# Performance work log

Hardware: AMD Instinct MI355X
Metric: run time of the kernel (lower is better)

Reference implementation:

```python
import jax, jax.numpy as jnp
import numpy as np

NUM_EMBED = 54012  # hardcoded self.num_nodes in GraphNet
IN_FEATS = 256
HID = 32           # hardcoded gcn1 output width
OUT_FEATS = 256
N_NODES = 65536
N_EDGES = 1048576
BATCH = 4096


def setup_inputs() -> dict:
    key = jax.random.key(0)
    ks = jax.random.split(key, 12)
    # graph structure (int args)
    idx = jax.random.randint(ks[0], (N_NODES,), 0, NUM_EMBED)
    src = jax.random.randint(ks[1], (N_EDGES,), 0, N_NODES)
    dst = jax.random.randint(ks[2], (N_EDGES,), 0, N_NODES)
    gene1_idx = jax.random.randint(ks[3], (BATCH,), 0, N_NODES)
    gene2_idx = jax.random.randint(ks[4], (BATCH,), 0, N_NODES)
    # learned parameters (xavier-ish scaling)
    embed = jax.random.normal(ks[5], (NUM_EMBED, IN_FEATS), jnp.float32) * (2.0 / (NUM_EMBED + IN_FEATS)) ** 0.5
    W1 = jax.random.normal(ks[6], (IN_FEATS, HID), jnp.float32) * (2.0 / (IN_FEATS + HID)) ** 0.5
    b1 = jnp.zeros((HID,), jnp.float32)
    W2 = jax.random.normal(ks[7], (HID, OUT_FEATS), jnp.float32) * (2.0 / (HID + OUT_FEATS)) ** 0.5
    b2 = jnp.zeros((OUT_FEATS,), jnp.float32)
    Wfc = jax.random.normal(ks[8], (2 * OUT_FEATS, OUT_FEATS), jnp.float32) * (2.0 / (3 * OUT_FEATS)) ** 0.5
    bfc = jnp.zeros((OUT_FEATS,), jnp.float32)
    return dict(idx=idx, src=src, dst=dst, gene1_idx=gene1_idx, gene2_idx=gene2_idx,
                embed=embed, W1=W1, b1=b1, W2=W2, b2=b2, Wfc=Wfc, bfc=bfc)


def _spmm_sum(feat, src, dst, n):
    # DGL copy_u + sum: out[v] = sum over edges (u->v) of feat[u]
    return jax.ops.segment_sum(feat[src], dst, num_segments=n)


def reference(idx, src, dst, gene1_idx, gene2_idx, embed, W1, b1, W2, b2, Wfc, bfc):
    n = idx.shape[0]
    feat = embed[idx]                              # [N, in_feats]
    # GCN layer 1: aggregate -> linear -> relu
    h = jax.nn.relu(_spmm_sum(feat, src, dst, n) @ W1 + b1)   # [N, 32]
    # GCN layer 2: aggregate -> linear (no activation)
    h2 = _spmm_sum(h, src, dst, n) @ W2 + b2                  # [N, out_feats]
    # per-graph SL gene pair gather + concat + linear + relu
    pair = jnp.concatenate([h2[gene1_idx], h2[gene2_idx]], axis=1)  # [B, 2*out_feats]
    return jax.nn.relu(pair @ Wfc + bfc)                      # [B, out_feats]
```

## Files before the change

### kernel.cpp

```cpp
#include <hip/hip_runtime.h>

#define IN_FEATS 256
#define HID 32
#define NUM_EMBED 54012
#define N_NODES 65536
#define N_EDGES 1048576
#define BATCH 4096

#define NR 256
#define NB 512
#define EPB (N_EDGES / NB)
#define PBCAP 32
#define HCAP 24
#define OVF_CAP 65536
#define GEMMB 844
#define NTILE 3376
#define W1P 280

typedef unsigned short u16t;
typedef unsigned int u32t;
typedef __attribute__((ext_vector_type(8))) short bf16x8;
typedef __attribute__((ext_vector_type(4))) float f32x4;

__device__ __forceinline__ float bf2f(u16t u) {
    return __uint_as_float(((u32t)u) << 16);
}
__device__ __forceinline__ u16t f2bf(float f) {
    u32t x = __float_as_uint(f);
    return (u16t)((x + 0x7FFFu + ((x >> 16) & 1u)) >> 16);
}
__device__ __forceinline__ u32t cvt_pk(float lo, float hi) {
    u32t r;
    asm("v_cvt_pk_bf16_f32 %0, %1, %2" : "=v"(r) : "v"(lo), "v"(hi));
    return r;
}

__device__ __forceinline__ float half_sum_bf(const int4* cell, int m,
                                             const u16t* __restrict__ feat1, int c) {
    int4 c0 = cell[0];
    u32t w[4] = {(u32t)c0.x, (u32t)c0.y, (u32t)c0.z, (u32t)c0.w};
    float va[8];
#pragma unroll
    for (int k = 0; k < 4; ++k) {
        va[2 * k + 0] = bf2f(feat1[((size_t)(w[k] & 0xFFFFu) << 5) + c]);
        va[2 * k + 1] = bf2f(feat1[((size_t)(w[k] >> 16) << 5) + c]);
    }
    float acc = 0.f;
#pragma unroll
    for (int j = 0; j < 8; ++j) acc += (m > j) ? va[j] : 0.f;
    if (m > 8) {
        int4 c1 = cell[1];
        u32t x[4] = {(u32t)c1.x, (u32t)c1.y, (u32t)c1.z, (u32t)c1.w};
        float vb[8];
#pragma unroll
        for (int k = 0; k < 4; ++k) {
            vb[2 * k + 0] = bf2f(feat1[((size_t)(x[k] & 0xFFFFu) << 5) + c]);
            vb[2 * k + 1] = bf2f(feat1[((size_t)(x[k] >> 16) << 5) + c]);
        }
#pragma unroll
        for (int j = 0; j < 8; ++j) acc += (m > 8 + j) ? vb[j] : 0.f;
        if (m > 16) {
            int4 c2 = cell[2];
            u32t y[4] = {(u32t)c2.x, (u32t)c2.y, (u32t)c2.z, (u32t)c2.w};
            float vc[8];
#pragma unroll
            for (int k = 0; k < 4; ++k) {
                vc[2 * k + 0] = bf2f(feat1[((size_t)(y[k] & 0xFFFFu) << 5) + c]);
                vc[2 * k + 1] = bf2f(feat1[((size_t)(y[k] >> 16) << 5) + c]);
            }
#pragma unroll
            for (int j = 0; j < 8; ++j) acc += (m > 16 + j) ? vc[j] : 0.f;
        }
    }
    return acc;
}

__device__ __forceinline__ float half_sum_f32(const int4* cell, int m,
                                              const float* __restrict__ agg1, int c) {
    int4 c0 = cell[0];
    u32t w[4] = {(u32t)c0.x, (u32t)c0.y, (u32t)c0.z, (u32t)c0.w};
    float va[8];
#pragma unroll
    for (int k = 0; k < 4; ++k) {
        va[2 * k + 0] = agg1[((size_t)(w[k] & 0xFFFFu) << 5) + c];
        va[2 * k + 1] = agg1[((size_t)(w[k] >> 16) << 5) + c];
    }
    float acc = 0.f;
#pragma unroll
    for (int j = 0; j < 8; ++j) acc += (m > j) ? va[j] : 0.f;
    if (m > 8) {
        int4 c1 = cell[1];
        u32t x[4] = {(u32t)c1.x, (u32t)c1.y, (u32t)c1.z, (u32t)c1.w};
        float vb[8];
#pragma unroll
        for (int k = 0; k < 4; ++k) {
            vb[2 * k + 0] = agg1[((size_t)(x[k] & 0xFFFFu) << 5) + c];
            vb[2 * k + 1] = agg1[((size_t)(x[k] >> 16) << 5) + c];
        }
#pragma unroll
        for (int j = 0; j < 8; ++j) acc += (m > 8 + j) ? vb[j] : 0.f;
        if (m > 16) {
            int4 c2 = cell[2];
            u32t y[4] = {(u32t)c2.x, (u32t)c2.y, (u32t)c2.z, (u32t)c2.w};
            float vc[8];
#pragma unroll
            for (int k = 0; k < 4; ++k) {
                vc[2 * k + 0] = agg1[((size_t)(y[k] & 0xFFFFu) << 5) + c];
                vc[2 * k + 1] = agg1[((size_t)(y[k] >> 16) << 5) + c];
            }
#pragma unroll
            for (int j = 0; j < 8; ++j) acc += (m > 16 + j) ? vc[j] : 0.f;
        }
    }
    return acc;
}

__global__ void k_phaseA(const float* __restrict__ embed, const float* __restrict__ W1,
                         u16t* __restrict__ tmpb,
                         const int* __restrict__ src, const int* __restrict__ dst,
                         u32t* __restrict__ subseg, u16t* __restrict__ hcnt,
                         int* __restrict__ ovf_cnt, int* __restrict__ ovf,
                         const float* __restrict__ W2, const float* __restrict__ b2,
                         const float* __restrict__ Wfc, const float* __restrict__ bfc,
                         float* __restrict__ M1, float* __restrict__ M2,
                         float* __restrict__ bias) {
    __shared__ __align__(16) char smem[32 * W1P * 2];
    int b = blockIdx.x;
    int t = threadIdx.x;

    if (b < NB) {
        int bb = b;
        u32t* hist = (u32t*)smem;
        u32t* cur  = hist + 256;
        u32t* epak = cur + 256;
        unsigned char* erng = (unsigned char*)(epak + EPB);
        hist[t] = 0;
        cur[t] = 0;
        __syncthreads();
        int base = bb * EPB;
#pragma unroll
        for (int k = 0; k < EPB / 256; ++k) {
            int i = k * 256 + t;
            int s = __builtin_nontemporal_load(&src[base + i]);
            int d = __builtin_nontemporal_load(&dst[base + i]);
            int r = d >> 8;
            epak[i] = (u32t)s | ((u32t)(d & 255) << 16);
            erng[i] = (unsigned char)r;
            atomicAdd(&hist[r], 1u);
        }
        __syncthreads();
        hcnt[t * NB + bb] = (u16t)min(hist[t], (u32t)PBCAP);
#pragma unroll
        for (int k = 0; k < EPB / 256; ++k) {
            int i = k * 256 + t;
            u32t w = epak[i];
            int r = erng[i];
            u32t p = atomicAdd(&cur[r], 1u);
            if (p < PBCAP) {
                subseg[((size_t)((u32t)r * NB + bb)) * PBCAP + p] = w;
            } else {
                int o = atomicAdd(ovf_cnt, 1);
                u32t dfull = ((u32t)r << 8) | (w >> 16);
                if (o < OVF_CAP) ovf[o] = (int)((w & 0xFFFFu) | (dfull << 16));
            }
        }
    } else if (b < NB + GEMMB) {
        u16t* w1t = (u16t*)smem;
        for (int i = t; i < IN_FEATS * HID; i += 256) {
            int k = i >> 5, c = i & 31;
            w1t[c * W1P + k] = f2bf(W1[i]);
        }
        __syncthreads();

        int lane = t & 63;
        int wv = t >> 6;
        int tile = (b - NB) * 4 + wv;
        if (tile >= NTILE) return;
        int r0 = tile * 16;

        int arow = min(r0 + (lane & 15), NUM_EMBED - 1);
        int kq = (lane >> 4) * 8;
        const float* Erow = embed + (size_t)arow * IN_FEATS + kq;

        int c = lane & 15;
        bf16x8 bf0[8], bf1[8];
        {
            const u16t* bp0 = w1t + (size_t)c * W1P + kq;
            const u16t* bp1 = w1t + (size_t)(c + 16) * W1P + kq;
#pragma unroll
            for (int kk = 0; kk < 8; ++kk) {
                bf0[kk] = *(const bf16x8*)(bp0 + kk * 32);
                bf1[kk] = *(const bf16x8*)(bp1 + kk * 32);
            }
        }

        f32x4 acc0 = {0.f, 0.f, 0.f, 0.f};
        f32x4 acc1 = {0.f, 0.f, 0.f, 0.f};
#pragma unroll
        for (int kk = 0; kk < 8; ++kk) {
            float4 p = *(const float4*)(Erow + kk * 32);
            float4 q = *(const float4*)(Erow + kk * 32 + 4);
            union { bf16x8 v; u32t u[4]; } a;
            a.u[0] = cvt_pk(p.x, p.y);
            a.u[1] = cvt_pk(p.z, p.w);
            a.u[2] = cvt_pk(q.x, q.y);
            a.u[3] = cvt_pk(q.z, q.w);
            acc0 = __builtin_amdgcn_mfma_f32_16x16x32_bf16(a.v, bf0[kk], acc0, 0, 0, 0);
            acc1 = __builtin_amdgcn_mfma_f32_16x16x32_bf16(a.v, bf1[kk], acc1, 0, 0, 0);
        }

        int rbase = r0 + (lane >> 4) * 4;
#pragma unroll
        for (int j = 0; j < 4; ++j) {
            int rr = rbase + j;
            if (rr < NUM_EMBED) {
                tmpb[(size_t)rr * HID + c]      = f2bf(acc0[j]);
                tmpb[(size_t)rr * HID + 16 + c] = f2bf(acc1[j]);
            }
        }
    } else {
        int r = b - NB - GEMMB;
        int c = t;
        if (r < 32) {
            float p0 = 0.f, p1 = 0.f, p2 = 0.f, p3 = 0.f;
#pragma unroll
            for (int j = 0; j < 256; j += 4) {
                p0 += W2[r * 256 + j + 0] * Wfc[(j + 0) * 256 + c];
                p1 += W2[r * 256 + j + 1] * Wfc[(j + 1) * 256 + c];
                p2 += W2[r * 256 + j + 2] * Wfc[(j + 2) * 256 + c];
                p3 += W2[r * 256 + j + 3] * Wfc[(j + 3) * 256 + c];
            }
            M1[r * 256 + c] = (p0 + p1) + (p2 + p3);
        } else if (r < 64) {
            int k = r - 32;
            float p0 = 0.f, p1 = 0.f, p2 = 0.f, p3 = 0.f;
#pragma unroll
            for (int j = 0; j < 256; j += 4) {
                p0 += W2[k * 256 + j + 0] * Wfc[(256 + j + 0) * 256 + c];
                p1 += W2[k * 256 + j + 1] * Wfc[(256 + j + 1) * 256 + c];
                p2 += W2[k * 256 + j + 2] * Wfc[(256 + j + 2) * 256 + c];
                p3 += W2[k * 256 + j + 3] * Wfc[(256 + j + 3) * 256 + c];
            }
            M2[k * 256 + c] = (p0 + p1) + (p2 + p3);
        } else {
            if (t == 0) *ovf_cnt = 0;
            float p0 = 0.f, p1 = 0.f;
#pragma unroll
            for (int j = 0; j < 256; j += 2) {
                p0 += b2[j + 0] * (Wfc[(j + 0) * 256 + c] + Wfc[(256 + j + 0) * 256 + c]);
                p1 += b2[j + 1] * (Wfc[(j + 1) * 256 + c] + Wfc[(256 + j + 1) * 256 + c]);
            }
            bias[c] = bfc[c] + p0 + p1;
        }
    }
}

__global__ void k_phaseB(const u32t* __restrict__ subseg, const u16t* __restrict__ hcnt,
                         u32t* __restrict__ cntAB, u16t* __restrict__ bins2,
                         int* __restrict__ ovf_cnt, int* __restrict__ ovf,
                         const u32t* __restrict__ tmpu, const int* __restrict__ idx,
                         u32t* __restrict__ feat1u) {
    __shared__ u16t cells[NR * HCAP];
    __shared__ u32t cl[NR];
    __shared__ u16t hc[NB / 2];
    int b = blockIdx.x;
    int t = threadIdx.x;
    if (b < 2 * NR) {
        int r = b >> 1, h = b & 1;
        for (int i = t; i < NR * HCAP / 2; i += 256) ((u32t*)cells)[i] = 0;
        cl[t] = 0;
        if (t < 128)
            ((u32t*)hc)[t] = ((const u32t*)(hcnt + (size_t)r * NB + h * 256))[t];
        __syncthreads();

        const u32t* segr = subseg + ((size_t)r * NB + h * 256) * PBCAP;
        for (int base_lin = 0; base_lin < 256 * PBCAP; base_lin += 2048) {
            u32t wbuf[8];
            int vld[8];
#pragma unroll
            for (int u = 0; u < 8; ++u) {
                int lin = base_lin + u * 256 + t;
                int bb = lin >> 5;
                int slot = lin & (PBCAP - 1);
                vld[u] = (slot < (int)hc[bb]);
                wbuf[u] = __builtin_nontemporal_load(&segr[lin]);
            }
#pragma unroll
            for (int u = 0; u < 8; ++u) {
                if (vld[u]) {
                    u32t w = wbuf[u];
                    int dl = (int)(w >> 16) & 255;
                    u32t p = atomicAdd(&cl[dl], 1u);
                    if (p < HCAP) {
                        cells[dl * HCAP + p] = (u16t)(w & 0xFFFFu);
                    } else {
                        int o = atomicAdd(ovf_cnt, 1);
                        u32t dfull = ((u32t)r << 8) | (u32t)dl;
                        if (o < OVF_CAP) ovf[o] = (int)((w & 0xFFFFu) | (dfull << 16));
                    }
                }
            }
        }
        __syncthreads();
        u32t* dst32 = (u32t*)(bins2) + ((size_t)h * N_NODES + ((size_t)r << 8)) * (HCAP / 2);
        for (int i = t; i < NR * HCAP / 2; i += 256)
            dst32[i] = ((const u32t*)cells)[i];
        ((u16t*)cntAB)[(((size_t)r << 8) + t) * 2 + h] = (u16t)min(cl[t], 65535u);
    } else {
        int i = (b - 2 * NR) * 256 + t;
        int n = i >> 4, j = i & 15;
        feat1u[((size_t)n << 4) + j] = tmpu[((size_t)idx[n] << 4) + j];
    }
}

__global__ void k_spmm1(const u16t* __restrict__ feat1,
                        const u32t* __restrict__ cntAB, const u16t* __restrict__ bins2,
                        const int* __restrict__ ovf_cnt, const int* __restrict__ ovf,
                        const float* __restrict__ b1, float* __restrict__ agg1) {
    int t = blockIdx.x * 256 + threadIdx.x;
    int v = t >> 5, c = t & 31;
    u32t cw = cntAB[v];
    int mA = min((int)(cw & 0xFFFFu), HCAP);
    int mB = min((int)(cw >> 16), HCAP);
    const int4* cellA = (const int4*)(bins2 + (size_t)v * HCAP);
    const int4* cellB = (const int4*)(bins2 + ((size_t)N_NODES + v) * HCAP);
    float acc = half_sum_bf(cellA, mA, feat1, c) + half_sum_bf(cellB, mB, feat1, c);

    int total = min(*ovf_cnt, OVF_CAP);
    for (int i = 0; i < total; ++i) {
        u32t e = (u32t)ovf[i];
        if ((e >> 16) == (u32t)v)
            acc += bf2f(feat1[((size_t)(e & 0xFFFFu) << 5) + c]);
    }
    agg1[t] = fmaxf(acc + b1[c], 0.f);
}

__global__ void k_tail(const float* __restrict__ agg1,
                       const u32t* __restrict__ cntAB, const u16t* __restrict__ bins2,
                       const int* __restrict__ ovf_cnt, const int* __restrict__ ovf,
                       const int* __restrict__ g1, const int* __restrict__ g2,
                       const float* __restrict__ M1, const float* __restrict__ M2,
                       const float* __restrict__ bias,
                       float* __restrict__ out) {
    __shared__ float a1s[8][HID];
    __shared__ float a2s[8][HID];
    int i0 = blockIdx.x * 8;
    int tid = threadIdx.x;
    int sg = tid >> 5, c = tid & 31;

    for (int side = 0; side < 2; ++side) {
        int slot = i0 + sg;
        int v = side ? g2[slot] : g1[slot];
        u32t cw = cntAB[v];
        int mA = min((int)(cw & 0xFFFFu), HCAP);
        int mB = min((int)(cw >> 16), HCAP);
        const int4* cellA = (const int4*)(bins2 + (size_t)v * HCAP);
        const int4* cellB = (const int4*)(bins2 + ((size_t)N_NODES + v) * HCAP);
        float acc = half_sum_f32(cellA, mA, agg1, c) + half_sum_f32(cellB, mB, agg1, c);

        int total = min(*ovf_cnt, OVF_CAP);
        for (int i = 0; i < total; ++i) {
            u32t e = (u32t)ovf[i];
            if ((e >> 16) == (u32t)v)
                acc += agg1[((size_t)(e & 0xFFFFu) << 5) + c];
        }
        if (side) a2s[sg][c] = acc;
        else      a1s[sg][c] = acc;
    }
    __syncthreads();

    int cc = tid;
    float acc[8];
#pragma unroll
    for (int q = 0; q < 8; ++q) acc[q] = bias[cc];
#pragma unroll
    for (int k = 0; k < HID; ++k) {
        float m1 = M1[k * 256 + cc];
        float m2 = M2[k * 256 + cc];
#pragma unroll
        for (int q = 0; q < 8; ++q)
            acc[q] += a1s[q][k] * m1 + a2s[q][k] * m2;
    }
#pragma unroll
    for (int q = 0; q < 8; ++q)
        out[(size_t)(i0 + q) * 256 + cc] = fmaxf(acc[q], 0.f);
}

extern "C" void kernel_launch(void* const* d_in, const int* in_sizes, int n_in,
                              void* d_out, int out_size, void* d_ws, size_t ws_size,
                              hipStream_t stream) {
    const int*   idx   = (const int*)d_in[0];
    const int*   src   = (const int*)d_in[1];
    const int*   dst   = (const int*)d_in[2];
    const int*   g1    = (const int*)d_in[3];
    const int*   g2    = (const int*)d_in[4];
    const float* embed = (const float*)d_in[5];
    const float* W1    = (const float*)d_in[6];
    const float* b1    = (const float*)d_in[7];
    const float* W2    = (const float*)d_in[8];
    const float* b2    = (const float*)d_in[9];
    const float* Wfc   = (const float*)d_in[10];
    const float* bfc   = (const float*)d_in[11];
    float* out = (float*)d_out;

    char* ws = (char*)d_ws;
    u16t*  tmpb     = (u16t*)ws;   ws += (size_t)NUM_EMBED * HID * 2 + 64;
    u16t*  feat1    = (u16t*)ws;   ws += (size_t)N_NODES * HID * 2;
    float* agg1     = (float*)ws;  ws += (size_t)N_NODES * HID * 4;
    float* M1       = (float*)ws;  ws += 32 * 256 * 4;
    float* M2       = (float*)ws;  ws += 32 * 256 * 4;
    float* bias     = (float*)ws;  ws += 256 * 4;
    u32t*  subseg   = (u32t*)ws;   ws += (size_t)NR * NB * PBCAP * 4;
    u16t*  hcnt     = (u16t*)ws;   ws += (size_t)NR * NB * 2;
    u32t*  cntAB    = (u32t*)ws;   ws += (size_t)N_NODES * 4;
    u16t*  bins2    = (u16t*)ws;   ws += (size_t)2 * N_NODES * HCAP * 2;
    int*   ovf_cnt  = (int*)ws;    ws += 64;
    int*   ovf      = (int*)ws;    ws += (size_t)OVF_CAP * 4;

    k_phaseA<<<NB + GEMMB + 65, 256, 0, stream>>>(embed, W1, tmpb,
                                                  src, dst, subseg, hcnt, ovf_cnt, ovf,
                                                  W2, b2, Wfc, bfc, M1, M2, bias);

    k_phaseB<<<2 * NR + (N_NODES * 16) / 256, 256, 0, stream>>>(subseg, hcnt,
                                                                cntAB, bins2,
                                                                ovf_cnt, ovf,
                                                                (const u32t*)tmpb, idx,
                                                                (u32t*)feat1);

    k_spmm1<<<(N_NODES * 32) / 256, 256, 0, stream>>>(feat1, cntAB, bins2,
                                                      ovf_cnt, ovf, b1, agg1);

    k_tail<<<BATCH / 8, 256, 0, stream>>>(agg1, cntAB, bins2, ovf_cnt, ovf,
                                          g1, g2, M1, M2, bias, out);
}
```

Before: 71.66 us.

## Stage edge buckets in LDS and write subsegments coalesced per block

Edge bucketing in phase A becomes a single pass. Each edge reserves a slot in a shared-memory cell array, and the whole per-block bucket image is then streamed to global memory with coalesced nontemporal stores, replacing scattered 4-byte global writes. The subsegment layout changes from range-major to block-major, the per-bucket capacity drops from 32 to 24, and phase B's reads are re-indexed to match. The intent is to cut uncoalesced write traffic and the separate histogram pass. In exchange, phase B reads become strided 96-byte chunks with non-power-of-two index math, and overflow becomes slightly more likely.

```diff
diff --git a/kernel.cpp b/kernel.cpp
--- a/kernel.cpp
+++ b/kernel.cpp
@@ -10,7 +10,7 @@
 #define NR 256
 #define NB 512
 #define EPB (N_EDGES / NB)
-#define PBCAP 32
+#define PBCAP 24
 #define HCAP 24
 #define OVF_CAP 65536
 #define GEMMB 844
@@ -124,17 +124,14 @@
                          const float* __restrict__ Wfc, const float* __restrict__ bfc,
                          float* __restrict__ M1, float* __restrict__ M2,
                          float* __restrict__ bias) {
-    __shared__ __align__(16) char smem[32 * W1P * 2];
+    __shared__ __align__(16) u32t smem4[256 + NR * PBCAP];
     int b = blockIdx.x;
     int t = threadIdx.x;
 
     if (b < NB) {
         int bb = b;
-        u32t* hist = (u32t*)smem;
-        u32t* cur  = hist + 256;
-        u32t* epak = cur + 256;
-        unsigned char* erng = (unsigned char*)(epak + EPB);
-        hist[t] = 0;
+        u32t* cur   = smem4;
+        u32t* cells = smem4 + 256;
         cur[t] = 0;
         __syncthreads();
         int base = bb * EPB;
@@ -144,28 +141,22 @@
             int s = __builtin_nontemporal_load(&src[base + i]);
             int d = __builtin_nontemporal_load(&dst[base + i]);
             int r = d >> 8;
-            epak[i] = (u32t)s | ((u32t)(d & 255) << 16);
-            erng[i] = (unsigned char)r;
-            atomicAdd(&hist[r], 1u);
-        }
-        __syncthreads();
-        hcnt[t * NB + bb] = (u16t)min(hist[t], (u32t)PBCAP);
-#pragma unroll
-        for (int k = 0; k < EPB / 256; ++k) {
-            int i = k * 256 + t;
-            u32t w = epak[i];
-            int r = erng[i];
+            u32t w = (u32t)s | ((u32t)(d & 255) << 16);
             u32t p = atomicAdd(&cur[r], 1u);
             if (p < PBCAP) {
-                subseg[((size_t)((u32t)r * NB + bb)) * PBCAP + p] = w;
+                cells[r * PBCAP + p] = w;
             } else {
                 int o = atomicAdd(ovf_cnt, 1);
-                u32t dfull = ((u32t)r << 8) | (w >> 16);
-                if (o < OVF_CAP) ovf[o] = (int)((w & 0xFFFFu) | (dfull << 16));
-            }
-        }
+                if (o < OVF_CAP) ovf[o] = (int)((u32t)s | ((u32t)d << 16));
+            }
+        }
+        __syncthreads();
+        hcnt[t * NB + bb] = (u16t)min(cur[t], (u32t)PBCAP);
+        u32t* dstp = subseg + (size_t)bb * (NR * PBCAP);
+        for (int i = t; i < NR * PBCAP; i += 256)
+            __builtin_nontemporal_store(cells[i], &dstp[i]);
     } else if (b < NB + GEMMB) {
-        u16t* w1t = (u16t*)smem;
+        u16t* w1t = (u16t*)smem4;
         for (int i = t; i < IN_FEATS * HID; i += 256) {
             int k = i >> 5, c = i & 31;
             w1t[c * W1P + k] = f2bf(W1[i]);
@@ -273,17 +264,18 @@
             ((u32t*)hc)[t] = ((const u32t*)(hcnt + (size_t)r * NB + h * 256))[t];
         __syncthreads();
 
-        const u32t* segr = subseg + ((size_t)r * NB + h * 256) * PBCAP;
+        const u32t* segbase = subseg + ((size_t)(h * 256) * NR + r) * PBCAP;
         for (int base_lin = 0; base_lin < 256 * PBCAP; base_lin += 2048) {
             u32t wbuf[8];
             int vld[8];
 #pragma unroll
             for (int u = 0; u < 8; ++u) {
                 int lin = base_lin + u * 256 + t;
-                int bb = lin >> 5;
-                int slot = lin & (PBCAP - 1);
+                int bb = lin / PBCAP;
+                int slot = lin - bb * PBCAP;
                 vld[u] = (slot < (int)hc[bb]);
-                wbuf[u] = __builtin_nontemporal_load(&segr[lin]);
+                wbuf[u] = __builtin_nontemporal_load(
+                    &segbase[(size_t)bb * (NR * PBCAP) + slot]);
             }
 #pragma unroll
             for (int u = 0; u < 8; ++u) {
@@ -410,7 +402,7 @@
     float* M1       = (float*)ws;  ws += 32 * 256 * 4;
     float* M2       = (float*)ws;  ws += 32 * 256 * 4;
     float* bias     = (float*)ws;  ws += 256 * 4;
-    u32t*  subseg   = (u32t*)ws;   ws += (size_t)NR * NB * PBCAP * 4;
+    u32t*  subseg   = (u32t*)ws;   ws += (size_t)NB * NR * PBCAP * 4;
     u16t*  hcnt     = (u16t*)ws;   ws += (size_t)NR * NB * 2;
     u32t*  cntAB    = (u32t*)ws;   ws += (size_t)N_NODES * 4;
     u16t*  bins2    = (u16t*)ws;   ws += (size_t)2 * N_NODES * HCAP * 2;
```

Result: faster. 69.63 us (-2.8%).
